# Performance work log

Measured on AMD Instinct MI355X. Metric: run time of the kernel, lower is better.

The kernel has to match this reference:

```python
import jax, jax.numpy as jnp
import numpy as np

D_MODEL = 2048
HEADDIM = 32
NHEADS = D_MODEL // HEADDIM  # 64
BLOCK = 256
EPS = 1e-4


def segsum(x):
    # x: (..., T) -> (..., T, T) stable segment sums, -inf above diagonal
    T = x.shape[-1]
    xe = jnp.broadcast_to(x[..., None], x.shape + (T,))  # (..., d, e)
    lower = jnp.tril(jnp.ones((T, T), dtype=bool), -1)
    xe = jnp.where(lower, xe, 0.0)
    s = jnp.cumsum(xe, axis=-2)
    incl = jnp.tril(jnp.ones((T, T), dtype=bool), 0)
    return jnp.where(incl, s, -jnp.inf)


def ssd_minimal_discrete(X, A, B, C, block_len):
    # X: (b, L, h, p); A: (b, L, h); B, C: (b, L, h, n). L % block_len == 0.
    b, Lm, h, p = X.shape
    c = Lm // block_len
    Xb = X.reshape(b, c, block_len, h, p)
    Bb = B.reshape(b, c, block_len, h, B.shape[-1])
    Cb = C.reshape(b, c, block_len, h, C.shape[-1])
    Ab = A.reshape(b, c, block_len, h).transpose(0, 3, 1, 2)  # (b, h, c, l)
    A_cumsum = jnp.cumsum(Ab, axis=-1)
    Lmat = jnp.exp(segsum(Ab))  # (b, h, c, l, s)
    # 1. intra-chunk (diagonal block) output
    Y_diag = jnp.einsum('bclhn,bcshn,bhcls,bcshp->bclhp', Cb, Bb, Lmat, Xb)
    # 2. per-chunk states
    decay_states = jnp.exp(A_cumsum[:, :, :, -1:] - A_cumsum)  # (b, h, c, l)
    states = jnp.einsum('bclhn,bhcl,bclhp->bchpn', Bb, decay_states, Xb)
    # 3. inter-chunk recurrence
    init = jnp.zeros_like(states[:, :1])
    states = jnp.concatenate([init, states], axis=1)  # (b, c+1, h, p, n)
    A_last = jnp.pad(A_cumsum[:, :, :, -1], ((0, 0), (0, 0), (1, 0)))  # (b, h, c+1)
    decay_chunk = jnp.exp(segsum(A_last))  # (b, h, c+1, c+1)
    new_states = jnp.einsum('bhzc,bchpn->bzhpn', decay_chunk, states)
    states_in, final_state = new_states[:, :-1], new_states[:, -1]
    # 4. state -> output within chunks
    state_decay_out = jnp.exp(A_cumsum)  # (b, h, c, l)
    Y_off = jnp.einsum('bclhn,bchpn,bhcl->bclhp', Cb, states_in, state_decay_out)
    Y = (Y_diag + Y_off).reshape(b, Lm, h, p)
    return Y, final_state


def setup_inputs() -> dict:
    key = jax.random.key(0)
    k1, k2 = jax.random.split(key)
    Bsz, Lfull, M = 2, 4096, 2048
    hidden_states = jax.random.normal(k1, (Bsz, M, D_MODEL), dtype=jnp.float32)
    # boundaries at even positions: exactly M boundaries per row, position 0 is a boundary
    boundary_mask = jnp.broadcast_to((jnp.arange(Lfull) % 2 == 0)[None, :], (Bsz, Lfull))
    boundary_prob = jax.random.uniform(k2, (Bsz, Lfull, 2), dtype=jnp.float32)
    mask = jnp.ones((Bsz, Lfull), dtype=bool)
    return {"hidden_states": hidden_states, "boundary_mask": boundary_mask,
            "boundary_prob": boundary_prob, "mask": mask}


def reference(hidden_states, boundary_mask, boundary_prob, mask):
    Bsz, Lfull = boundary_mask.shape
    M = hidden_states.shape[1]
    # select boundary-position probabilities, in order, first M
    p = jnp.clip(boundary_prob[..., -1].astype(jnp.float32), EPS, 1.0 - EPS)
    token_idx = jnp.arange(Lfull)[None, :] + (~boundary_mask).astype(jnp.int32) * Lfull
    order = jnp.argsort(token_idx, axis=1, stable=True)
    p_sel = jnp.take_along_axis(p, order[:, :M], axis=1)  # (B, M)
    dt = jnp.log(1.0 / (1.0 - p_sel))
    x = hidden_states.astype(jnp.float32) / dt[..., None]
    Xr = x.reshape(Bsz, M, NHEADS, HEADDIM)
    A_dt = -jnp.broadcast_to(dt[:, :, None], (Bsz, M, NHEADS))  # A = -1, A*dt
    B_ssd = jnp.broadcast_to(p_sel[:, :, None, None], (Bsz, M, NHEADS, 1))
    C_ssd = jnp.ones_like(B_ssd)
    out, _ = ssd_minimal_discrete(Xr, A_dt, B_ssd, C_ssd, BLOCK)
    out = out.reshape(Bsz, M, D_MODEL)
    # plug back: each uncompressed token reads the EMA value of its chunk
    plug = jnp.cumsum(boundary_mask.astype(jnp.int32), axis=1) - 1  # (B, L)
    out = jnp.take_along_axis(out, plug[:, :, None], axis=1)  # (B, L, d_model)
    return out
```

## Files before the change

kernel.cpp:

```cpp
#include <hip/hip_runtime.h>
#include <math.h>

#define BSZ    2
#define LFULL  4096
#define MLEN   2048
#define DMODEL 2048
#define CLIP_EPS 1e-4f
#define CCH    256
#define TCH    8

typedef float f4 __attribute__((ext_vector_type(4)));

__global__ __launch_bounds__(256) void k1_prep(
    const int* __restrict__ bmask_raw, const float* __restrict__ bprob,
    int* __restrict__ Ls, int* __restrict__ Le,
    float* __restrict__ wA, float* __restrict__ eA,
    float* __restrict__ cde, float* __restrict__ Pc)
{
  const int b   = blockIdx.x;
  const int tid = threadIdx.x;

  __shared__ int   s_cnt[257];
  __shared__ int   s_mode;
  __shared__ int   s_ntrue;
  __shared__ int   s_sel[MLEN];
  __shared__ float s_e[MLEN];

  if (tid == 0) {
    unsigned w0 = ((const unsigned*)bmask_raw)[0];
    s_mode = (w0 <= 1u) ? 1 : 0;
  }
  __syncthreads();
  const int mode = s_mode;
  const unsigned char* bmask_u8 = (const unsigned char*)bmask_raw;

  const int PER = LFULL / 256;
  const int base = tid * PER;

  int cnt = 0;
  for (int i = 0; i < PER; ++i) {
    const int L = base + i;
    const int v = mode ? (bmask_raw[b * LFULL + L] != 0)
                       : (bmask_u8[b * LFULL + L] != 0);
    cnt += v;
  }
  s_cnt[tid] = cnt;
  __syncthreads();

  if (tid < 64) {
    const int j = tid * 4;
    const int c0 = s_cnt[j], c1 = s_cnt[j + 1], c2 = s_cnt[j + 2], c3 = s_cnt[j + 3];
    const int mysum = c0 + c1 + c2 + c3;
    int incl = mysum;
    #pragma unroll
    for (int off = 1; off < 64; off <<= 1) {
      const int v = __shfl_up(incl, off, 64);
      if (tid >= off) incl += v;
    }
    const int excl = incl - mysum;
    s_cnt[j]     = excl;
    s_cnt[j + 1] = excl + c0;
    s_cnt[j + 2] = excl + c0 + c1;
    s_cnt[j + 3] = excl + c0 + c1 + c2;
    if (tid == 63) { s_cnt[256] = incl; s_ntrue = incl; }
  }
  __syncthreads();
  const int ntrue = s_ntrue;

  int trun = s_cnt[tid];
  for (int i = 0; i < PER; ++i) {
    const int L = base + i;
    const int v = mode ? (bmask_raw[b * LFULL + L] != 0)
                       : (bmask_u8[b * LFULL + L] != 0);
    if (v) {
      if (trun < MLEN) s_sel[trun] = L;
      ++trun;
    } else {
      const int f = L - trun;
      const int slot = ntrue + f;
      if (slot < MLEN) s_sel[slot] = L;
    }
  }
  __syncthreads();

  for (int j = tid; j < MLEN; j += 256) {
    const int L = s_sel[j];
    float p = bprob[((size_t)b * LFULL + L) * 2 + 1];
    p = fminf(fmaxf(p, CLIP_EPS), 1.0f - CLIP_EPS);
    const float dt = -log1pf(-p);
    wA[b * MLEN + j] = p / dt;
    const float e = 1.0f - p;
    eA[b * MLEN + j] = e;
    s_e[j] = e;
  }
  __syncthreads();

  {
    const int c = tid;
    const int o = c * TCH;
    float run = 1.0f;
    #pragma unroll
    for (int i = 0; i < TCH; ++i) {
      run *= s_e[o + i];
      cde[b * MLEN + o + i] = run;
    }
    Pc[b * CCH + c] = run;
  }

  const int nb = (ntrue < MLEN) ? ntrue : MLEN;
  for (int j = tid; j < MLEN; j += 256) {
    int ls, le;
    if (nb == 0) {
      ls = (j == 0) ? 0 : LFULL;
      le = (j == 0) ? LFULL : LFULL;
    } else if (j < nb) {
      ls = (j == 0) ? 0 : s_sel[j];
      le = (j == nb - 1) ? LFULL : s_sel[j + 1];
    } else {
      ls = LFULL; le = LFULL;
    }
    Ls[b * MLEN + j] = ls;
    Le[b * MLEN + j] = le;
  }
}

__global__ __launch_bounds__(256) void k2_states(
    const float* __restrict__ hid, const float* __restrict__ wA,
    const float* __restrict__ eA, float* __restrict__ S)
{
  const int tid = threadIdx.x;
  const int c = blockIdx.y;
  const int b = blockIdx.z;

  __shared__ float s_w[TCH], s_e[TCH];
  if (tid < TCH)            s_w[tid]       = wA[b * MLEN + c * TCH + tid];
  else if (tid < 2 * TCH)   s_e[tid - TCH] = eA[b * MLEN + c * TCH + (tid - TCH)];
  __syncthreads();

  const int d4 = blockIdx.x * 256 + tid;
  const f4* xp = (const f4*)hid + ((size_t)(b * MLEN + c * TCH) * DMODEL >> 2) + d4;

  f4 st = {0.f, 0.f, 0.f, 0.f};
  #pragma unroll
  for (int t = 0; t < TCH; ++t) {
    const f4 x = xp[(size_t)t * (DMODEL / 4)];
    const float w = s_w[t], e = s_e[t];
    st.x = fmaf(e, st.x, w * x.x);
    st.y = fmaf(e, st.y, w * x.y);
    st.z = fmaf(e, st.z, w * x.z);
    st.w = fmaf(e, st.w, w * x.w);
  }
  ((f4*)S)[((size_t)(b * CCH + c) * DMODEL >> 2) + d4] = st;
}

__global__ __launch_bounds__(256) void k25_scan(
    const float* __restrict__ Pc, float* __restrict__ S)
{
  const int c  = threadIdx.x;
  const int d4 = blockIdx.x;
  const int b  = blockIdx.y;

  __shared__ float sP[CCH];
  __shared__ f4    sS[CCH];

  f4* Sf4 = (f4*)S;
  const size_t idx = ((size_t)(b * CCH + c) * DMODEL >> 2) + d4;

  sP[c] = Pc[b * CCH + c];
  sS[c] = Sf4[idx];
  __syncthreads();

  #pragma unroll
  for (int dstep = 1; dstep < CCH; dstep <<= 1) {
    float pd = 1.0f;
    f4 sd = {0.f, 0.f, 0.f, 0.f};
    if (c >= dstep) { pd = sP[c - dstep]; sd = sS[c - dstep]; }
    __syncthreads();
    if (c >= dstep) {
      f4 cur = sS[c];
      const float pc = sP[c];
      cur.x = fmaf(pc, sd.x, cur.x);
      cur.y = fmaf(pc, sd.y, cur.y);
      cur.z = fmaf(pc, sd.z, cur.z);
      cur.w = fmaf(pc, sd.w, cur.w);
      sS[c] = cur;
      sP[c] = pc * pd;
    }
    __syncthreads();
  }

  f4 g = {0.f, 0.f, 0.f, 0.f};
  if (c > 0) g = sS[c - 1];
  Sf4[idx] = g;
}

__global__ __launch_bounds__(256) void k3_out(
    const float* __restrict__ hid, const float* __restrict__ wA,
    const float* __restrict__ eA, const float* __restrict__ cde,
    const float* __restrict__ G,
    const int* __restrict__ Ls, const int* __restrict__ Le,
    float* __restrict__ out)
{
  const int tid = threadIdx.x;
  const int c = blockIdx.y;
  const int b = blockIdx.z;

  __shared__ float s_w[TCH], s_e[TCH], s_c[TCH];
  __shared__ int   s_ls[TCH], s_le[TCH];
  const int o = b * MLEN + c * TCH;
  if (tid < TCH)          { s_w[tid] = wA[o + tid];  s_ls[tid] = Ls[o + tid]; }
  else if (tid < 2 * TCH) { const int t = tid - TCH;     s_e[t] = eA[o + t]; s_le[t] = Le[o + t]; }
  else if (tid < 3 * TCH) { const int t = tid - 2 * TCH; s_c[t] = cde[o + t]; }
  __syncthreads();

  const int d4 = blockIdx.x * 256 + tid;

  const f4 H = ((const f4*)G)[((size_t)(b * CCH + c) * DMODEL >> 2) + d4];

  const f4* xp = (const f4*)hid + ((size_t)(b * MLEN + c * TCH) * DMODEL >> 2) + d4;
  f4*       op = (f4*)out + ((size_t)b * LFULL * DMODEL >> 2) + d4;

  f4 st = {0.f, 0.f, 0.f, 0.f};
  #pragma unroll
  for (int t = 0; t < TCH; ++t) {
    const f4 x = xp[(size_t)t * (DMODEL / 4)];
    const float w = s_w[t], e = s_e[t], cd = s_c[t];
    st.x = fmaf(e, st.x, w * x.x);
    st.y = fmaf(e, st.y, w * x.y);
    st.z = fmaf(e, st.z, w * x.z);
    st.w = fmaf(e, st.w, w * x.w);
    f4 y;
    y.x = fmaf(cd, H.x, st.x);
    y.y = fmaf(cd, H.y, st.y);
    y.z = fmaf(cd, H.z, st.z);
    y.w = fmaf(cd, H.w, st.w);
    const int ls = s_ls[t], le = s_le[t];
    for (int L = ls; L < le; ++L) {
      __builtin_nontemporal_store(y, op + (size_t)L * (DMODEL / 4));
    }
  }
}

extern "C" void kernel_launch(void* const* d_in, const int* in_sizes, int n_in,
                              void* d_out, int out_size, void* d_ws, size_t ws_size,
                              hipStream_t stream) {
  const float* hid   = (const float*)d_in[0];
  const int*   bmask = (const int*)d_in[1];
  const float* bprob = (const float*)d_in[2];
  float*       out   = (float*)d_out;

  char* ws = (char*)d_ws;
  const size_t SZI = (size_t)BSZ * MLEN * sizeof(int);
  const size_t SZF = (size_t)BSZ * MLEN * sizeof(float);
  int*   Ls  = (int*)(ws);
  int*   Le  = (int*)(ws + SZI);
  float* wA  = (float*)(ws + 2 * SZI);
  float* eA  = (float*)(ws + 2 * SZI + SZF);
  float* cde = (float*)(ws + 2 * SZI + 2 * SZF);
  float* Pc  = (float*)(ws + 2 * SZI + 3 * SZF);
  float* S   = (float*)(ws + 2 * SZI + 3 * SZF + 4096);

  k1_prep<<<dim3(BSZ), dim3(256), 0, stream>>>(bmask, bprob, Ls, Le, wA, eA, cde, Pc);

  dim3 grid(DMODEL / 1024, CCH, BSZ);
  k2_states<<<grid, dim3(256), 0, stream>>>(hid, wA, eA, S);

  k25_scan<<<dim3(DMODEL / 4, BSZ), dim3(256), 0, stream>>>(Pc, S);

  k3_out<<<grid, dim3(256), 0, stream>>>(hid, wA, eA, cde, S, Ls, Le, out);
}
```

Before: 128.4 us.

## Fuse chunk-state, inter-chunk scan and output kernels into one kernel

```diff
diff --git a/kernel.cpp b/kernel.cpp
--- a/kernel.cpp
+++ b/kernel.cpp
@@ -124,117 +124,73 @@
   }
 }
 
-__global__ __launch_bounds__(256) void k2_states(
+__global__ __launch_bounds__(1024, 4) void k2b_fused(
     const float* __restrict__ hid, const float* __restrict__ wA,
-    const float* __restrict__ eA, float* __restrict__ S)
+    const float* __restrict__ eA, const float* __restrict__ cde,
+    const float* __restrict__ Pc,
+    const int* __restrict__ Ls, const int* __restrict__ Le,
+    float* __restrict__ out)
 {
   const int tid = threadIdx.x;
-  const int c = blockIdx.y;
-  const int b = blockIdx.z;
-
-  __shared__ float s_w[TCH], s_e[TCH];
-  if (tid < TCH)            s_w[tid]       = wA[b * MLEN + c * TCH + tid];
-  else if (tid < 2 * TCH)   s_e[tid - TCH] = eA[b * MLEN + c * TCH + (tid - TCH)];
-  __syncthreads();
-
-  const int d4 = blockIdx.x * 256 + tid;
-  const f4* xp = (const f4*)hid + ((size_t)(b * MLEN + c * TCH) * DMODEL >> 2) + d4;
-
+  const int j   = tid & 3;
+  const int c   = tid >> 2;
+  const int bx  = blockIdx.x;
+  const int b   = blockIdx.y;
+
+  __shared__ float sP[CCH];
+  __shared__ f4    sS[CCH][4];
+
+  const int d4 = bx * 4 + j;
+  const int o  = b * MLEN + c * TCH;
+
+  const f4* xp = (const f4*)hid + ((size_t)o * DMODEL >> 2) + d4;
+  f4 xr[TCH];
   f4 st = {0.f, 0.f, 0.f, 0.f};
   #pragma unroll
   for (int t = 0; t < TCH; ++t) {
     const f4 x = xp[(size_t)t * (DMODEL / 4)];
-    const float w = s_w[t], e = s_e[t];
+    const float w = wA[o + t], e = eA[o + t];
     st.x = fmaf(e, st.x, w * x.x);
     st.y = fmaf(e, st.y, w * x.y);
     st.z = fmaf(e, st.z, w * x.z);
     st.w = fmaf(e, st.w, w * x.w);
-  }
-  ((f4*)S)[((size_t)(b * CCH + c) * DMODEL >> 2) + d4] = st;
-}
-
-__global__ __launch_bounds__(256) void k25_scan(
-    const float* __restrict__ Pc, float* __restrict__ S)
-{
-  const int c  = threadIdx.x;
-  const int d4 = blockIdx.x;
-  const int b  = blockIdx.y;
-
-  __shared__ float sP[CCH];
-  __shared__ f4    sS[CCH];
-
-  f4* Sf4 = (f4*)S;
-  const size_t idx = ((size_t)(b * CCH + c) * DMODEL >> 2) + d4;
-
-  sP[c] = Pc[b * CCH + c];
-  sS[c] = Sf4[idx];
-  __syncthreads();
-
-  #pragma unroll
+    xr[t] = st;
+  }
+  sS[c][j] = st;
+  if (j == 0) sP[c] = Pc[b * CCH + c];
+  __syncthreads();
+
   for (int dstep = 1; dstep < CCH; dstep <<= 1) {
+    const float pc = sP[c];
     float pd = 1.0f;
     f4 sd = {0.f, 0.f, 0.f, 0.f};
-    if (c >= dstep) { pd = sP[c - dstep]; sd = sS[c - dstep]; }
+    if (c >= dstep) { pd = sP[c - dstep]; sd = sS[c - dstep][j]; }
     __syncthreads();
     if (c >= dstep) {
-      f4 cur = sS[c];
-      const float pc = sP[c];
+      f4 cur = sS[c][j];
       cur.x = fmaf(pc, sd.x, cur.x);
       cur.y = fmaf(pc, sd.y, cur.y);
       cur.z = fmaf(pc, sd.z, cur.z);
       cur.w = fmaf(pc, sd.w, cur.w);
-      sS[c] = cur;
-      sP[c] = pc * pd;
+      sS[c][j] = cur;
+      if (j == 0) sP[c] = pc * pd;
     }
     __syncthreads();
   }
 
-  f4 g = {0.f, 0.f, 0.f, 0.f};
-  if (c > 0) g = sS[c - 1];
-  Sf4[idx] = g;
-}
-
-__global__ __launch_bounds__(256) void k3_out(
-    const float* __restrict__ hid, const float* __restrict__ wA,
-    const float* __restrict__ eA, const float* __restrict__ cde,
-    const float* __restrict__ G,
-    const int* __restrict__ Ls, const int* __restrict__ Le,
-    float* __restrict__ out)
-{
-  const int tid = threadIdx.x;
-  const int c = blockIdx.y;
-  const int b = blockIdx.z;
-
-  __shared__ float s_w[TCH], s_e[TCH], s_c[TCH];
-  __shared__ int   s_ls[TCH], s_le[TCH];
-  const int o = b * MLEN + c * TCH;
-  if (tid < TCH)          { s_w[tid] = wA[o + tid];  s_ls[tid] = Ls[o + tid]; }
-  else if (tid < 2 * TCH) { const int t = tid - TCH;     s_e[t] = eA[o + t]; s_le[t] = Le[o + t]; }
-  else if (tid < 3 * TCH) { const int t = tid - 2 * TCH; s_c[t] = cde[o + t]; }
-  __syncthreads();
-
-  const int d4 = blockIdx.x * 256 + tid;
-
-  const f4 H = ((const f4*)G)[((size_t)(b * CCH + c) * DMODEL >> 2) + d4];
-
-  const f4* xp = (const f4*)hid + ((size_t)(b * MLEN + c * TCH) * DMODEL >> 2) + d4;
-  f4*       op = (f4*)out + ((size_t)b * LFULL * DMODEL >> 2) + d4;
-
-  f4 st = {0.f, 0.f, 0.f, 0.f};
+  f4 H = {0.f, 0.f, 0.f, 0.f};
+  if (c > 0) H = sS[c - 1][j];
+
+  f4* op = (f4*)out + ((size_t)b * LFULL * DMODEL >> 2) + d4;
   #pragma unroll
   for (int t = 0; t < TCH; ++t) {
-    const f4 x = xp[(size_t)t * (DMODEL / 4)];
-    const float w = s_w[t], e = s_e[t], cd = s_c[t];
-    st.x = fmaf(e, st.x, w * x.x);
-    st.y = fmaf(e, st.y, w * x.y);
-    st.z = fmaf(e, st.z, w * x.z);
-    st.w = fmaf(e, st.w, w * x.w);
+    const float cd = cde[o + t];
     f4 y;
-    y.x = fmaf(cd, H.x, st.x);
-    y.y = fmaf(cd, H.y, st.y);
-    y.z = fmaf(cd, H.z, st.z);
-    y.w = fmaf(cd, H.w, st.w);
-    const int ls = s_ls[t], le = s_le[t];
+    y.x = fmaf(cd, H.x, xr[t].x);
+    y.y = fmaf(cd, H.y, xr[t].y);
+    y.z = fmaf(cd, H.z, xr[t].z);
+    y.w = fmaf(cd, H.w, xr[t].w);
+    const int ls = Ls[o + t], le = Le[o + t];
     for (int L = ls; L < le; ++L) {
       __builtin_nontemporal_store(y, op + (size_t)L * (DMODEL / 4));
     }
@@ -258,14 +214,9 @@
   float* eA  = (float*)(ws + 2 * SZI + SZF);
   float* cde = (float*)(ws + 2 * SZI + 2 * SZF);
   float* Pc  = (float*)(ws + 2 * SZI + 3 * SZF);
-  float* S   = (float*)(ws + 2 * SZI + 3 * SZF + 4096);
 
   k1_prep<<<dim3(BSZ), dim3(256), 0, stream>>>(bmask, bprob, Ls, Le, wA, eA, cde, Pc);
 
-  dim3 grid(DMODEL / 1024, CCH, BSZ);
-  k2_states<<<grid, dim3(256), 0, stream>>>(hid, wA, eA, S);
-
-  k25_scan<<<dim3(DMODEL / 4, BSZ), dim3(256), 0, stream>>>(Pc, S);
-
-  k3_out<<<grid, dim3(256), 0, stream>>>(hid, wA, eA, cde, S, Ls, Le, out);
+  k2b_fused<<<dim3(DMODEL / 16, BSZ), dim3(1024), 0, stream>>>(
+      hid, wA, eA, cde, Pc, Ls, Le, out);
 }
```

New measurement: 118.6 us. 7.6% less time.
